# Kernel tuning notes

Measured on AMD Instinct MI355X. Metric: run time of the kernel, lower is better.

## Reference

```python
import jax, jax.numpy as jnp
import numpy as np

D_MODEL = 1024
NUM_HEADS = 16
D_K = D_MODEL // NUM_HEADS
D_FF = 4096
EPS = 1e-6


def setup_inputs() -> dict:
    key = jax.random.key(0)
    ks = jax.random.split(key, 12)
    B, S = 4, 1024
    s = 1.0 / np.sqrt(D_MODEL)
    return {
        "x": jax.random.normal(ks[0], (B, S, D_MODEL), dtype=jnp.float32),
        "ln1_g": jnp.ones((D_MODEL,), jnp.float32),
        "ln1_b": jnp.zeros((D_MODEL,), jnp.float32),
        "wq": jax.random.normal(ks[1], (D_MODEL, D_MODEL), jnp.float32) * s,
        "wk": jax.random.normal(ks[2], (D_MODEL, D_MODEL), jnp.float32) * s,
        "wv": jax.random.normal(ks[3], (D_MODEL, D_MODEL), jnp.float32) * s,
        "wo": jax.random.normal(ks[4], (D_MODEL, D_MODEL), jnp.float32) * s,
        "ln2_g": jnp.ones((D_MODEL,), jnp.float32),
        "ln2_b": jnp.zeros((D_MODEL,), jnp.float32),
        "w1": jax.random.normal(ks[5], (D_MODEL, D_FF), jnp.float32) * s,
        "b1": jnp.zeros((D_FF,), jnp.float32),
        "w2": jax.random.normal(ks[6], (D_FF, D_MODEL), jnp.float32) * (1.0 / np.sqrt(D_FF)),
        "b2": jnp.zeros((D_MODEL,), jnp.float32),
    }


def _layernorm(x, g, b):
    mu = jnp.mean(x, axis=-1, keepdims=True)
    var = jnp.var(x, axis=-1, keepdims=True)
    return (x - mu) * jax.lax.rsqrt(var + EPS) * g + b


def _mha(x, wq, wk, wv, wo):
    B, S, _ = x.shape
    # project and split heads: [B,S,D] -> [B,H,S,Dk]
    q = (x @ wq).reshape(B, S, NUM_HEADS, D_K).transpose(0, 2, 1, 3)
    k = (x @ wk).reshape(B, S, NUM_HEADS, D_K).transpose(0, 2, 1, 3)
    v = (x @ wv).reshape(B, S, NUM_HEADS, D_K).transpose(0, 2, 1, 3)
    scores = jnp.einsum("bhqd,bhkd->bhqk", q, k) / np.sqrt(D_K).astype(np.float32)
    attn = jax.nn.softmax(scores, axis=-1)  # no mask: source forwards mask=None
    out = jnp.einsum("bhqk,bhkd->bhqd", attn, v)
    out = out.transpose(0, 2, 1, 3).reshape(B, S, D_MODEL)
    return out @ wo


def reference(x, ln1_g, ln1_b, wq, wk, wv, wo, ln2_g, ln2_b, w1, b1, w2, b2):
    x1 = _layernorm(x, ln1_g, ln1_b)
    x = x + _mha(x1, wq, wk, wv, wo)  # dropout identity (eval)
    x2 = _layernorm(x, ln2_g, ln2_b)
    ffn = jax.nn.relu(x2 @ w1 + b1) @ w2 + b2
    return x + ffn
```

## Files before the change

### kernel.cpp

```cpp
#include <hip/hip_runtime.h>

typedef __bf16 bf16;
typedef __bf16 bf16x8 __attribute__((ext_vector_type(8)));
typedef __bf16 bf16x4 __attribute__((ext_vector_type(4)));
typedef float f32x4 __attribute__((ext_vector_type(4)));

__device__ __forceinline__ void gload_lds16(const void* g, void* l) {
  __builtin_amdgcn_global_load_lds(
      (const __attribute__((address_space(1))) unsigned int*)g,
      (__attribute__((address_space(3))) unsigned int*)l, 16, 0, 0);
}

__global__ __launch_bounds__(256) void transpose_cast(const float* __restrict__ src,
                                                      bf16* __restrict__ dst,
                                                      int R, int C) {
  __shared__ float tile[32][33];
  const int tx = threadIdx.x & 31, ty = threadIdx.x >> 5;
  const int c0 = blockIdx.x * 32, r0 = blockIdx.y * 32;
#pragma unroll
  for (int i = 0; i < 4; i++)
    tile[ty + i * 8][tx] = src[(size_t)(r0 + ty + i * 8) * C + c0 + tx];
  __syncthreads();
#pragma unroll
  for (int i = 0; i < 4; i++)
    dst[(size_t)(c0 + ty + i * 8) * R + r0 + tx] = (bf16)tile[tx][ty + i * 8];
}

__global__ __launch_bounds__(256) void ln_kernel(const float* __restrict__ x,
                                                 const float* __restrict__ g,
                                                 const float* __restrict__ b,
                                                 bf16* __restrict__ y) {
  const int w = threadIdx.x >> 6, lane = threadIdx.x & 63;
  const int row = blockIdx.x * 4 + w;
  const float* xr = x + (size_t)row * 1024;
  float4 v[4];
  float s = 0.f, sq = 0.f;
#pragma unroll
  for (int c = 0; c < 4; c++) {
    v[c] = *reinterpret_cast<const float4*>(xr + c * 256 + lane * 4);
    s += v[c].x + v[c].y + v[c].z + v[c].w;
    sq += v[c].x * v[c].x + v[c].y * v[c].y + v[c].z * v[c].z + v[c].w * v[c].w;
  }
#pragma unroll
  for (int d = 32; d >= 1; d >>= 1) {
    s += __shfl_xor(s, d, 64);
    sq += __shfl_xor(sq, d, 64);
  }
  const float mu = s * (1.f / 1024.f);
  const float rs = rsqrtf(sq * (1.f / 1024.f) - mu * mu + 1e-6f);
#pragma unroll
  for (int c = 0; c < 4; c++) {
    float4 gv = *reinterpret_cast<const float4*>(g + c * 256 + lane * 4);
    float4 bv = *reinterpret_cast<const float4*>(b + c * 256 + lane * 4);
    bf16x4 ov;
    ov[0] = (bf16)((v[c].x - mu) * rs * gv.x + bv.x);
    ov[1] = (bf16)((v[c].y - mu) * rs * gv.y + bv.y);
    ov[2] = (bf16)((v[c].z - mu) * rs * gv.z + bv.z);
    ov[3] = (bf16)((v[c].w - mu) * rs * gv.w + bv.w);
    *reinterpret_cast<bf16x4*>(y + (size_t)row * 1024 + c * 256 + lane * 4) = ov;
  }
}

__global__ __launch_bounds__(256) void reduce_ln_kernel(const bf16* __restrict__ p0,
                                                        const bf16* __restrict__ p1,
                                                        const float* __restrict__ x,
                                                        const float* __restrict__ g,
                                                        const float* __restrict__ b,
                                                        float* __restrict__ xres,
                                                        bf16* __restrict__ y) {
  const int w = threadIdx.x >> 6, lane = threadIdx.x & 63;
  const int row = blockIdx.x * 4 + w;
  const size_t rb = (size_t)row * 1024;
  float4 v[4];
  float s = 0.f, sq = 0.f;
#pragma unroll
  for (int c = 0; c < 4; c++) {
    const int off = c * 256 + lane * 4;
    float4 xv = *reinterpret_cast<const float4*>(x + rb + off);
    bf16x4 a0 = *reinterpret_cast<const bf16x4*>(p0 + rb + off);
    bf16x4 a1 = *reinterpret_cast<const bf16x4*>(p1 + rb + off);
    v[c].x = xv.x + (float)a0[0] + (float)a1[0];
    v[c].y = xv.y + (float)a0[1] + (float)a1[1];
    v[c].z = xv.z + (float)a0[2] + (float)a1[2];
    v[c].w = xv.w + (float)a0[3] + (float)a1[3];
    *reinterpret_cast<float4*>(xres + rb + off) = v[c];
    s += v[c].x + v[c].y + v[c].z + v[c].w;
    sq += v[c].x * v[c].x + v[c].y * v[c].y + v[c].z * v[c].z + v[c].w * v[c].w;
  }
#pragma unroll
  for (int d = 32; d >= 1; d >>= 1) {
    s += __shfl_xor(s, d, 64);
    sq += __shfl_xor(sq, d, 64);
  }
  const float mu = s * (1.f / 1024.f);
  const float rs = rsqrtf(sq * (1.f / 1024.f) - mu * mu + 1e-6f);
#pragma unroll
  for (int c = 0; c < 4; c++) {
    const int off = c * 256 + lane * 4;
    float4 gv = *reinterpret_cast<const float4*>(g + off);
    float4 bv = *reinterpret_cast<const float4*>(b + off);
    bf16x4 ov;
    ov[0] = (bf16)((v[c].x - mu) * rs * gv.x + bv.x);
    ov[1] = (bf16)((v[c].y - mu) * rs * gv.y + bv.y);
    ov[2] = (bf16)((v[c].z - mu) * rs * gv.z + bv.z);
    ov[3] = (bf16)((v[c].w - mu) * rs * gv.w + bv.w);
    *reinterpret_cast<bf16x4*>(y + rb + off) = ov;
  }
}

__global__ __launch_bounds__(256) void reduce_out_kernel(const bf16* __restrict__ p0,
                                                         const bf16* __restrict__ p1,
                                                         const bf16* __restrict__ p2,
                                                         const bf16* __restrict__ p3,
                                                         const float* __restrict__ bias,
                                                         const float* __restrict__ xres,
                                                         float* __restrict__ out) {
  const size_t i = ((size_t)blockIdx.x * 256 + threadIdx.x) * 8;
  const int col = (int)(i & 1023);
  bf16x8 a0 = *reinterpret_cast<const bf16x8*>(p0 + i);
  bf16x8 a1 = *reinterpret_cast<const bf16x8*>(p1 + i);
  bf16x8 a2 = *reinterpret_cast<const bf16x8*>(p2 + i);
  bf16x8 a3 = *reinterpret_cast<const bf16x8*>(p3 + i);
  float4 r0 = *reinterpret_cast<const float4*>(xres + i);
  float4 r1 = *reinterpret_cast<const float4*>(xres + i + 4);
  float4 b0 = *reinterpret_cast<const float4*>(bias + col);
  float4 b1 = *reinterpret_cast<const float4*>(bias + col + 4);
  float4 o0, o1;
  o0.x = r0.x + b0.x + (float)a0[0] + (float)a1[0] + (float)a2[0] + (float)a3[0];
  o0.y = r0.y + b0.y + (float)a0[1] + (float)a1[1] + (float)a2[1] + (float)a3[1];
  o0.z = r0.z + b0.z + (float)a0[2] + (float)a1[2] + (float)a2[2] + (float)a3[2];
  o0.w = r0.w + b0.w + (float)a0[3] + (float)a1[3] + (float)a2[3] + (float)a3[3];
  o1.x = r1.x + b1.x + (float)a0[4] + (float)a1[4] + (float)a2[4] + (float)a3[4];
  o1.y = r1.y + b1.y + (float)a0[5] + (float)a1[5] + (float)a2[5] + (float)a3[5];
  o1.z = r1.z + b1.z + (float)a0[6] + (float)a1[6] + (float)a2[6] + (float)a3[6];
  o1.w = r1.w + b1.w + (float)a0[7] + (float)a1[7] + (float)a2[7] + (float)a3[7];
  *reinterpret_cast<float4*>(out + i) = o0;
  *reinterpret_cast<float4*>(out + i + 4) = o1;
}

template <int EPI>
__global__ __launch_bounds__(256) void gemm_bt(const bf16* __restrict__ A,
                                               const bf16* __restrict__ Bt,
                                               void* __restrict__ Cout,
                                               const float* __restrict__ bias,
                                               int M, int N, int K, int gy, int gxy,
                                               int Kc) {
  __shared__ __align__(16) bf16 As[2][128][32];
  __shared__ __align__(16) bf16 Bs[2][128][32];
  const int tid = threadIdx.x;
  const int w = tid >> 6, lane = tid & 63;
  const int wr = w >> 1, wc = w & 1;

  const int nwg = gridDim.x;
  const int cpx = nwg >> 3;
  const int swz = (blockIdx.x & 7) * cpx + (blockIdx.x >> 3);
  const int chunk = swz / gxy, rem = swz % gxy;
  const int gpc = gy << 3;
  const int band = rem / gpc, r2 = rem % gpc;
  const int bm = (band * 8 + (r2 & 7)) * 128;
  const int bn = (r2 >> 3) * 128;

  f32x4 acc[4][4] = {};
  const int r4 = lane >> 2;
  const int c8 = (lane & 3) * 8;
  const bf16* Ag = A + (size_t)(bm + w * 32 + r4) * K + chunk * Kc + c8;
  const bf16* Bg = Bt + (size_t)(bn + w * 32 + r4) * K + chunk * Kc + c8;
  const int fr = lane & 15, fo = (lane >> 4) * 8;

#define STAGE(buf, k0)                                                 \
  do {                                                                 \
    gload_lds16(Ag + (k0), &As[buf][w * 32][0]);                       \
    gload_lds16(Ag + (size_t)16 * K + (k0), &As[buf][w * 32 + 16][0]); \
    gload_lds16(Bg + (k0), &Bs[buf][w * 32][0]);                       \
    gload_lds16(Bg + (size_t)16 * K + (k0), &Bs[buf][w * 32 + 16][0]); \
  } while (0)

  const int nt = Kc >> 5;
  STAGE(0, 0);
  __syncthreads();
  int cur = 0;
  for (int t = 0; t < nt; ++t) {
    if (t + 1 < nt) STAGE(cur ^ 1, (t + 1) << 5);
    bf16x8 af[4], bfr[4];
#pragma unroll
    for (int m = 0; m < 4; m++)
      af[m] = *reinterpret_cast<const bf16x8*>(&As[cur][wr * 64 + m * 16 + fr][fo]);
#pragma unroll
    for (int n = 0; n < 4; n++)
      bfr[n] = *reinterpret_cast<const bf16x8*>(&Bs[cur][wc * 64 + n * 16 + fr][fo]);
#pragma unroll
    for (int m = 0; m < 4; m++)
#pragma unroll
      for (int n = 0; n < 4; n++)
        acc[m][n] = __builtin_amdgcn_mfma_f32_16x16x32_bf16(af[m], bfr[n], acc[m][n], 0, 0, 0);
    __syncthreads();
    cur ^= 1;
  }
#undef STAGE

  bf16* outp = (bf16*)Cout + (EPI == 3 ? (size_t)chunk * M * N : 0);
  const int cr = (lane >> 4) * 4, cc = lane & 15;
#pragma unroll
  for (int m = 0; m < 4; m++) {
#pragma unroll
    for (int n = 0; n < 4; n++) {
      const int row = bm + wr * 64 + m * 16 + cr;
      const int col = bn + wc * 64 + n * 16 + cc;
#pragma unroll
      for (int r = 0; r < 4; r++) {
        const float va = acc[m][n][r];
        const size_t idx = (size_t)(row + r) * N + col;
        if (EPI == 0 || EPI == 3) {
          outp[idx] = (bf16)va;
        } else {
          const float t = va + bias[col];
          outp[idx] = (bf16)(t > 0.f ? t : 0.f);
        }
      }
    }
  }
}

template <int EPI>
__global__ __launch_bounds__(512, 2) void gemm256(const bf16* __restrict__ A,
                                                  const bf16* __restrict__ Bt,
                                                  void* __restrict__ Cout,
                                                  const float* __restrict__ bias,
                                                  int M, int N, int K, int gy, int gxy,
                                                  int Kc) {
  __shared__ __align__(16) bf16 As[2][256][64];
  __shared__ __align__(16) bf16 Bs[2][256][64];
  const int tid = threadIdx.x;
  const int w = tid >> 6, lane = tid & 63;
  const int wm = w >> 2, wn = w & 3;
  const int fr = lane & 15, g = lane >> 4;

  const int nwg = gridDim.x;
  const int cpx = nwg >> 3;
  const int swz = (blockIdx.x & 7) * cpx + (blockIdx.x >> 3);
  const int chunk = swz / gxy, rem = swz % gxy;
  const int gpc = gy << 3;
  const int band = rem / gpc, r2 = rem % gpc;
  const int bm = (band * 8 + (r2 & 7)) * 256;
  const int bn = (r2 >> 3) * 256;

  const bf16* Ab = A + (size_t)bm * K;
  const bf16* Bb = Bt + (size_t)bn * K;

  const int lr = lane >> 3;
  const int sle = ((lane & 7) ^ lr) * 8;
  const int rB0 = w * 16;
  const int rB1 = 128 + w * 16;
  const int rA0 = wm * 128 + wn * 16;
  const int rA1 = wm * 128 + 64 + wn * 16;

  char* AsB = (char*)&As[0][0][0];
  char* BsB = (char*)&Bs[0][0][0];
  const int rowA = (wm * 128 + fr) * 128;
  const int rowB = (wn * 64 + fr) * 128;
  const int colk0 = (g * 16) ^ ((fr & 7) << 4);
  const int colk1 = (64 + g * 16) ^ ((fr & 7) << 4);

  f32x4 acc[8][4] = {};

#define SG8(base, r0, kb, ldsrow)                                           \
  do {                                                                      \
    gload_lds16(base + (size_t)((r0) + lr) * K + (kb) + sle, (ldsrow));     \
    gload_lds16(base + (size_t)((r0) + 8 + lr) * K + (kb) + sle,            \
                (char*)(ldsrow) + 1024);                                    \
  } while (0)

  const int nt = Kc >> 6;
  const int koff = chunk * Kc;

  SG8(Bb, rB0, koff, BsB + rB0 * 128);
  SG8(Bb, rB1, koff, BsB + rB1 * 128);
  SG8(Ab, rA0, koff, AsB + rA0 * 128);
  SG8(Ab, rA1, koff, AsB + rA1 * 128);

#define PHASE_BODY(p, mb)                                                     \
  {                                                                           \
    if ((p) == 0) {                                                           \
      _Pragma("unroll") for (int nf = 0; nf < 4; nf++) {                      \
        bfr[nf][0] = *(const bf16x8*)(Br + rowB + nf * 2048 + colk0);         \
        bfr[nf][1] = *(const bf16x8*)(Br + rowB + nf * 2048 + colk1);         \
      }                                                                       \
    }                                                                         \
    af[0][0] = *(const bf16x8*)(Ar + rowA + (mb)*2048 + colk0);               \
    af[0][1] = *(const bf16x8*)(Ar + rowA + (mb)*2048 + colk1);               \
    af[1][0] = *(const bf16x8*)(Ar + rowA + ((mb) + 1) * 2048 + colk0);       \
    af[1][1] = *(const bf16x8*)(Ar + rowA + ((mb) + 1) * 2048 + colk1);       \
    if (pre) {                                                                \
      if ((p) == 0) SG8(Bb, rB0, kb2, Bw + rB0 * 128);                        \
      if ((p) == 1) SG8(Bb, rB1, kb2, Bw + rB1 * 128);                        \
      if ((p) == 2) SG8(Ab, rA0, kb2, Aw + rA0 * 128);                        \
      if ((p) == 3) SG8(Ab, rA1, kb2, Aw + rA1 * 128);                        \
    }                                                                         \
    __builtin_amdgcn_s_setprio(1);                                            \
    _Pragma("unroll") for (int m2 = 0; m2 < 2; m2++)                          \
        _Pragma("unroll") for (int nf = 0; nf < 4; nf++) {                    \
      acc[(mb) + m2][nf] = __builtin_amdgcn_mfma_f32_16x16x32_bf16(           \
          af[m2][0], bfr[nf][0], acc[(mb) + m2][nf], 0, 0, 0);                \
      acc[(mb) + m2][nf] = __builtin_amdgcn_mfma_f32_16x16x32_bf16(           \
          af[m2][1], bfr[nf][1], acc[(mb) + m2][nf], 0, 0, 0);                \
    }                                                                         \
    __builtin_amdgcn_s_setprio(0);                                            \
  }

  int buf = 0;
  for (int kt = 0; kt < nt; ++kt) {
    char* Ar = AsB + buf * 32768;
    char* Br = BsB + buf * 32768;
    char* Aw = AsB + (buf ^ 1) * 32768;
    char* Bw = BsB + (buf ^ 1) * 32768;
    const bool pre = (kt + 1) < nt;
    const int kb2 = koff + (kt + 1) * 64;
    bf16x8 bfr[4][2];
    bf16x8 af[2][2];

    asm volatile("s_waitcnt vmcnt(2)" ::: "memory");
    __builtin_amdgcn_s_barrier();
    PHASE_BODY(0, 0)

    if (pre) asm volatile("s_waitcnt vmcnt(4)" ::: "memory");
    else     asm volatile("s_waitcnt vmcnt(2)" ::: "memory");
    __builtin_amdgcn_s_barrier();
    PHASE_BODY(1, 2)

    if (pre) asm volatile("s_waitcnt vmcnt(4)" ::: "memory");
    else     asm volatile("s_waitcnt vmcnt(0)" ::: "memory");
    __builtin_amdgcn_s_barrier();
    PHASE_BODY(2, 4)

    if (pre) asm volatile("s_waitcnt vmcnt(6)" ::: "memory");
    else     asm volatile("s_waitcnt vmcnt(0)" ::: "memory");
    __builtin_amdgcn_s_barrier();
    PHASE_BODY(3, 6)

    buf ^= 1;
  }
#undef PHASE_BODY
#undef SG8

  bf16* outp = (bf16*)Cout + (EPI == 3 ? (size_t)chunk * M * N : 0);
  const int cr = g * 4;
#pragma unroll
  for (int mf = 0; mf < 8; mf++) {
#pragma unroll
    for (int nf = 0; nf < 4; nf++) {
      const int row = bm + wm * 128 + mf * 16 + cr;
      const int col = bn + wn * 64 + nf * 16 + fr;
#pragma unroll
      for (int r = 0; r < 4; r++) {
        const float va = acc[mf][nf][r];
        const size_t idx = (size_t)(row + r) * N + col;
        if (EPI == 3) {
          outp[idx] = (bf16)va;
        } else {
          const float t = va + bias[col];
          outp[idx] = (bf16)(t > 0.f ? t : 0.f);
        }
      }
    }
  }
}

__global__ __launch_bounds__(256) void attn_kernel(const bf16* __restrict__ Q,
                                                   const bf16* __restrict__ K,
                                                   const bf16* __restrict__ V,
                                                   bf16* __restrict__ O, int ld) {
  __shared__ __align__(16) bf16 Ks[2][64][64];
  __shared__ __align__(16) bf16 Vt[2][64][64];
  __shared__ __align__(16) bf16 Pl[4][32][64];
  const int tid = threadIdx.x;
  const int w = tid >> 6, l = tid & 63;
  const int lo = l & 15, g = l >> 4;
  const int sw = (lo & 7) << 3;

  const int id = blockIdx.x;
  const int bh = id & 63, qb = id >> 6;
  const int b = bh >> 4, h = bh & 15;
  const int hoff = h * 64;
  const size_t rowQ = (size_t)b * 1024 + qb * 128 + w * 32;
  const size_t rowKV0 = (size_t)b * 1024;

  bf16x8 qfr[2][2];
#pragma unroll
  for (int qi = 0; qi < 2; qi++)
#pragma unroll
    for (int ds = 0; ds < 2; ds++)
      qfr[qi][ds] = *reinterpret_cast<const bf16x8*>(
          Q + (rowQ + qi * 16 + lo) * ld + hoff + ds * 32 + g * 8);

  const float c = 0.18033688f;
  float m[2] = {-1e30f, -1e30f}, lsum[2] = {0.f, 0.f};
  f32x4 o[4][2] = {};

  {
#pragma unroll
    for (int i = 0; i < 2; i++) {
      const int idx = tid + i * 256;
      const int row = idx >> 3, cch = idx & 7;
      gload_lds16(K + (rowKV0 + row) * ld + hoff + ((cch ^ (row & 7)) << 3),
                  &Ks[0][row][cch << 3]);
    }
    const bf16* vp = V + (rowKV0 + l) * ld + hoff + w * 16;
    bf16x8 va = *reinterpret_cast<const bf16x8*>(vp);
    bf16x8 vb = *reinterpret_cast<const bf16x8*>(vp + 8);
#pragma unroll
    for (int j = 0; j < 8; j++) Vt[0][w * 16 + j][l ^ (j << 3)] = va[j];
#pragma unroll
    for (int j = 0; j < 8; j++) Vt[0][w * 16 + 8 + j][l ^ (j << 3)] = vb[j];
  }
  __syncthreads();

  int bb = 0;
  for (int kt = 0; kt < 16; kt++) {
    bf16x8 va, vb;
    const bool more = (kt + 1) < 16;
    if (more) {
      const size_t rkv = rowKV0 + (kt + 1) * 64;
#pragma unroll
      for (int i = 0; i < 2; i++) {
        const int idx = tid + i * 256;
        const int row = idx >> 3, cch = idx & 7;
        gload_lds16(K + (rkv + row) * ld + hoff + ((cch ^ (row & 7)) << 3),
                    &Ks[bb ^ 1][row][cch << 3]);
      }
      const bf16* vp = V + (rkv + l) * ld + hoff + w * 16;
      va = *reinterpret_cast<const bf16x8*>(vp);
      vb = *reinterpret_cast<const bf16x8*>(vp + 8);
    }

    f32x4 sa[4][2] = {};
#pragma unroll
    for (int ds = 0; ds < 2; ds++) {
      bf16x8 kf[4];
#pragma unroll
      for (int kfi = 0; kfi < 4; kfi++)
        kf[kfi] = *reinterpret_cast<const bf16x8*>(&Ks[bb][kfi * 16 + lo][(ds * 32 + g * 8) ^ sw]);
#pragma unroll
      for (int kfi = 0; kfi < 4; kfi++)
#pragma unroll
        for (int qi = 0; qi < 2; qi++)
          sa[kfi][qi] = __builtin_amdgcn_mfma_f32_16x16x32_bf16(kf[kfi], qfr[qi][ds], sa[kfi][qi], 0, 0, 0);
    }

#pragma unroll
    for (int qi = 0; qi < 2; qi++) {
      float m0 = fmaxf(fmaxf(sa[0][qi][0], sa[0][qi][1]), fmaxf(sa[0][qi][2], sa[0][qi][3]));
      float m1 = fmaxf(fmaxf(sa[1][qi][0], sa[1][qi][1]), fmaxf(sa[1][qi][2], sa[1][qi][3]));
      float m2 = fmaxf(fmaxf(sa[2][qi][0], sa[2][qi][1]), fmaxf(sa[2][qi][2], sa[2][qi][3]));
      float m3 = fmaxf(fmaxf(sa[3][qi][0], sa[3][qi][1]), fmaxf(sa[3][qi][2], sa[3][qi][3]));
      float mx = fmaxf(fmaxf(m0, m1), fmaxf(m2, m3));
      mx = fmaxf(mx, __shfl_xor(mx, 16));
      mx = fmaxf(mx, __shfl_xor(mx, 32));
      const float mn = fmaxf(m[qi], mx);
      const float sc = exp2f((m[qi] - mn) * c);
      const float mc = mn * c;
      m[qi] = mn;
      float p[16];
#pragma unroll
      for (int kfi = 0; kfi < 4; kfi++)
#pragma unroll
        for (int r = 0; r < 4; r++)
          p[kfi * 4 + r] = exp2f(fmaf(sa[kfi][qi][r], c, -mc));
      float s0 = (p[0] + p[1]) + (p[2] + p[3]);
      float s1 = (p[4] + p[5]) + (p[6] + p[7]);
      float s2 = (p[8] + p[9]) + (p[10] + p[11]);
      float s3 = (p[12] + p[13]) + (p[14] + p[15]);
      float sum = (s0 + s1) + (s2 + s3);
      sum += __shfl_xor(sum, 16);
      sum += __shfl_xor(sum, 32);
      lsum[qi] = lsum[qi] * sc + sum;
#pragma unroll
      for (int df = 0; df < 4; df++)
#pragma unroll
        for (int r = 0; r < 4; r++) o[df][qi][r] *= sc;
#pragma unroll
      for (int kfi = 0; kfi < 4; kfi++) {
        bf16x4 pk;
        pk[0] = (bf16)p[kfi * 4 + 0];
        pk[1] = (bf16)p[kfi * 4 + 1];
        pk[2] = (bf16)p[kfi * 4 + 2];
        pk[3] = (bf16)p[kfi * 4 + 3];
        *reinterpret_cast<bf16x4*>(&Pl[w][qi * 16 + lo][(kfi * 16 + g * 4) ^ sw]) = pk;
      }
    }

#pragma unroll
    for (int ks = 0; ks < 2; ks++) {
      bf16x8 pf[2], vf[4];
#pragma unroll
      for (int qi = 0; qi < 2; qi++)
        pf[qi] = *reinterpret_cast<const bf16x8*>(&Pl[w][qi * 16 + lo][(ks * 32 + g * 8) ^ sw]);
#pragma unroll
      for (int df = 0; df < 4; df++)
        vf[df] = *reinterpret_cast<const bf16x8*>(&Vt[bb][df * 16 + lo][(ks * 32 + g * 8) ^ sw]);
#pragma unroll
      for (int df = 0; df < 4; df++)
#pragma unroll
        for (int qi = 0; qi < 2; qi++)
          o[df][qi] = __builtin_amdgcn_mfma_f32_16x16x32_bf16(vf[df], pf[qi], o[df][qi], 0, 0, 0);
    }

    if (more) {
#pragma unroll
      for (int j = 0; j < 8; j++) Vt[bb ^ 1][w * 16 + j][l ^ (j << 3)] = va[j];
#pragma unroll
      for (int j = 0; j < 8; j++) Vt[bb ^ 1][w * 16 + 8 + j][l ^ (j << 3)] = vb[j];
    }
    __syncthreads();
    bb ^= 1;
  }

#pragma unroll
  for (int qi = 0; qi < 2; qi++) {
    const float rl = 1.f / lsum[qi];
#pragma unroll
    for (int df = 0; df < 4; df++) {
      bf16x4 ov;
#pragma unroll
      for (int r = 0; r < 4; r++) ov[r] = (bf16)(o[df][qi][r] * rl);
      *reinterpret_cast<bf16x4*>(&Pl[w][qi * 16 + lo][(df * 16 + g * 4) ^ sw]) = ov;
    }
  }
  const int row = l >> 1;
  const int swr = (row & 7) << 3;
#pragma unroll
  for (int i = 0; i < 4; i++) {
    const int c2 = (l & 1) * 4 + i;
    bf16x8 ov = *reinterpret_cast<const bf16x8*>(&Pl[w][row][(c2 * 8) ^ swr]);
    *reinterpret_cast<bf16x8*>(O + (rowQ + row) * 1024 + hoff + c2 * 8) = ov;
  }
}

extern "C" void kernel_launch(void* const* d_in, const int* in_sizes, int n_in,
                              void* d_out, int out_size, void* d_ws, size_t ws_size,
                              hipStream_t stream) {
  const float* x     = (const float*)d_in[0];
  const float* ln1_g = (const float*)d_in[1];
  const float* ln1_b = (const float*)d_in[2];
  const float* wq    = (const float*)d_in[3];
  const float* wk    = (const float*)d_in[4];
  const float* wv    = (const float*)d_in[5];
  const float* wo    = (const float*)d_in[6];
  const float* ln2_g = (const float*)d_in[7];
  const float* ln2_b = (const float*)d_in[8];
  const float* w1    = (const float*)d_in[9];
  const float* b1    = (const float*)d_in[10];
  const float* w2    = (const float*)d_in[11];
  const float* b2    = (const float*)d_in[12];

  const size_t MB = 1ull << 20;
  char* ws = (char*)d_ws;
  bf16* wTqkv = (bf16*)(ws + 0 * MB);
  bf16* wTo   = (bf16*)(ws + 6 * MB);
  bf16* wT1   = (bf16*)(ws + 8 * MB);
  bf16* wT2   = (bf16*)(ws + 16 * MB);
  bf16* x1    = (bf16*)(ws + 24 * MB);
  bf16* qkv   = (bf16*)(ws + 32 * MB);
  float* xres = (float*)(ws + 56 * MB);
  bf16* h1    = (bf16*)(ws + 72 * MB);
  bf16* attn  = x1;
  bf16* x2    = qkv;
  bf16* pOp   = (bf16*)(ws + 40 * MB);
  bf16* pF    = (bf16*)(ws + 24 * MB);

  const dim3 TB(256);

  transpose_cast<<<dim3(32, 32), TB, 0, stream>>>(wq, wTqkv, 1024, 1024);
  transpose_cast<<<dim3(32, 32), TB, 0, stream>>>(wk, wTqkv + 1024 * 1024, 1024, 1024);
  transpose_cast<<<dim3(32, 32), TB, 0, stream>>>(wv, wTqkv + 2048 * 1024, 1024, 1024);
  transpose_cast<<<dim3(32, 32), TB, 0, stream>>>(wo, wTo, 1024, 1024);
  transpose_cast<<<dim3(128, 32), TB, 0, stream>>>(w1, wT1, 1024, 4096);
  transpose_cast<<<dim3(32, 128), TB, 0, stream>>>(w2, wT2, 4096, 1024);

  ln_kernel<<<1024, TB, 0, stream>>>(x, ln1_g, ln1_b, x1);

  gemm_bt<0><<<768, TB, 0, stream>>>(x1, wTqkv, qkv, nullptr, 4096, 3072, 1024, 24, 768, 1024);

  attn_kernel<<<512, TB, 0, stream>>>(qkv, qkv + 1024, qkv + 2048, attn, 3072);

  gemm_bt<3><<<512, TB, 0, stream>>>(attn, wTo, pOp, nullptr, 4096, 1024, 1024, 8, 256, 512);

  reduce_ln_kernel<<<1024, TB, 0, stream>>>(pOp, pOp + 4096 * 1024, x, ln2_g, ln2_b, xres, x2);

  gemm256<2><<<256, dim3(512), 0, stream>>>(x2, wT1, h1, b1, 4096, 4096, 1024, 16, 256, 1024);

  gemm256<3><<<256, dim3(512), 0, stream>>>(h1, wT2, pF, nullptr, 4096, 1024, 4096, 4, 64, 1024);

  reduce_out_kernel<<<2048, TB, 0, stream>>>(pF, pF + 4096 * 1024, pF + 2 * 4096 * 1024,
                                             pF + 3 * 4096 * 1024, b2, xres, (float*)d_out);
}
```

Measured before the change: 219.9 us.

## Use 8 waves per attention block and skip unneeded softmax rescaling

Attention blocks now run 512 threads (8 waves), each wave handling 16 query rows instead of 32. The K/V tile loads are split across more threads and register pressure per wave drops, which is meant to raise occupancy and latency hiding. The online softmax also updates the running max and rescales the accumulators only when some lane's new max exceeds the stored one by more than a threshold. This saves the exp and multiply work in most iterations, but lets exponent arguments grow up to a bounded amount.

```diff
diff --git a/kernel.cpp b/kernel.cpp
--- a/kernel.cpp
+++ b/kernel.cpp
@@ -365,13 +365,13 @@
   }
 }
 
-__global__ __launch_bounds__(256) void attn_kernel(const bf16* __restrict__ Q,
-                                                   const bf16* __restrict__ K,
-                                                   const bf16* __restrict__ V,
-                                                   bf16* __restrict__ O, int ld) {
+__global__ __launch_bounds__(512, 4) void attn_kernel(const bf16* __restrict__ Q,
+                                                      const bf16* __restrict__ K,
+                                                      const bf16* __restrict__ V,
+                                                      bf16* __restrict__ O, int ld) {
   __shared__ __align__(16) bf16 Ks[2][64][64];
   __shared__ __align__(16) bf16 Vt[2][64][64];
-  __shared__ __align__(16) bf16 Pl[4][32][64];
+  __shared__ __align__(16) bf16 Pl[8][16][64];
   const int tid = threadIdx.x;
   const int w = tid >> 6, l = tid & 63;
   const int lo = l & 15, g = l >> 4;
@@ -381,58 +381,43 @@
   const int bh = id & 63, qb = id >> 6;
   const int b = bh >> 4, h = bh & 15;
   const int hoff = h * 64;
-  const size_t rowQ = (size_t)b * 1024 + qb * 128 + w * 32;
+  const size_t rowQ = (size_t)b * 1024 + qb * 128 + w * 16;
   const size_t rowKV0 = (size_t)b * 1024;
 
-  bf16x8 qfr[2][2];
-#pragma unroll
-  for (int qi = 0; qi < 2; qi++)
-#pragma unroll
-    for (int ds = 0; ds < 2; ds++)
-      qfr[qi][ds] = *reinterpret_cast<const bf16x8*>(
-          Q + (rowQ + qi * 16 + lo) * ld + hoff + ds * 32 + g * 8);
+  const int srow = tid >> 3, scch = tid & 7;
+  const int vcb = w * 8;
+
+  bf16x8 qfr[2];
+#pragma unroll
+  for (int ds = 0; ds < 2; ds++)
+    qfr[ds] = *reinterpret_cast<const bf16x8*>(
+        Q + (rowQ + lo) * ld + hoff + ds * 32 + g * 8);
 
   const float c = 0.18033688f;
-  float m[2] = {-1e30f, -1e30f}, lsum[2] = {0.f, 0.f};
-  f32x4 o[4][2] = {};
+  float m = -1e30f, lsum = 0.f;
+  f32x4 o[4] = {};
 
   {
-#pragma unroll
-    for (int i = 0; i < 2; i++) {
-      const int idx = tid + i * 256;
-      const int row = idx >> 3, cch = idx & 7;
-      gload_lds16(K + (rowKV0 + row) * ld + hoff + ((cch ^ (row & 7)) << 3),
-                  &Ks[0][row][cch << 3]);
-    }
-    const bf16* vp = V + (rowKV0 + l) * ld + hoff + w * 16;
-    bf16x8 va = *reinterpret_cast<const bf16x8*>(vp);
-    bf16x8 vb = *reinterpret_cast<const bf16x8*>(vp + 8);
-#pragma unroll
-    for (int j = 0; j < 8; j++) Vt[0][w * 16 + j][l ^ (j << 3)] = va[j];
-#pragma unroll
-    for (int j = 0; j < 8; j++) Vt[0][w * 16 + 8 + j][l ^ (j << 3)] = vb[j];
+    gload_lds16(K + (rowKV0 + srow) * ld + hoff + ((scch ^ (srow & 7)) << 3),
+                &Ks[0][w * 8][0]);
+    bf16x8 vv = *reinterpret_cast<const bf16x8*>(V + (rowKV0 + l) * ld + hoff + vcb);
+#pragma unroll
+    for (int j = 0; j < 8; j++) Vt[0][vcb + j][l ^ (j << 3)] = vv[j];
   }
   __syncthreads();
 
   int bb = 0;
   for (int kt = 0; kt < 16; kt++) {
-    bf16x8 va, vb;
+    bf16x8 vv;
     const bool more = (kt + 1) < 16;
     if (more) {
       const size_t rkv = rowKV0 + (kt + 1) * 64;
-#pragma unroll
-      for (int i = 0; i < 2; i++) {
-        const int idx = tid + i * 256;
-        const int row = idx >> 3, cch = idx & 7;
-        gload_lds16(K + (rkv + row) * ld + hoff + ((cch ^ (row & 7)) << 3),
-                    &Ks[bb ^ 1][row][cch << 3]);
-      }
-      const bf16* vp = V + (rkv + l) * ld + hoff + w * 16;
-      va = *reinterpret_cast<const bf16x8*>(vp);
-      vb = *reinterpret_cast<const bf16x8*>(vp + 8);
-    }
-
-    f32x4 sa[4][2] = {};
+      gload_lds16(K + (rkv + srow) * ld + hoff + ((scch ^ (srow & 7)) << 3),
+                  &Ks[bb ^ 1][w * 8][0]);
+      vv = *reinterpret_cast<const bf16x8*>(V + (rkv + l) * ld + hoff + vcb);
+    }
+
+    f32x4 sa[4] = {};
 #pragma unroll
     for (int ds = 0; ds < 2; ds++) {
       bf16x8 kf[4];
@@ -441,97 +426,84 @@
         kf[kfi] = *reinterpret_cast<const bf16x8*>(&Ks[bb][kfi * 16 + lo][(ds * 32 + g * 8) ^ sw]);
 #pragma unroll
       for (int kfi = 0; kfi < 4; kfi++)
-#pragma unroll
-        for (int qi = 0; qi < 2; qi++)
-          sa[kfi][qi] = __builtin_amdgcn_mfma_f32_16x16x32_bf16(kf[kfi], qfr[qi][ds], sa[kfi][qi], 0, 0, 0);
-    }
-
-#pragma unroll
-    for (int qi = 0; qi < 2; qi++) {
-      float m0 = fmaxf(fmaxf(sa[0][qi][0], sa[0][qi][1]), fmaxf(sa[0][qi][2], sa[0][qi][3]));
-      float m1 = fmaxf(fmaxf(sa[1][qi][0], sa[1][qi][1]), fmaxf(sa[1][qi][2], sa[1][qi][3]));
-      float m2 = fmaxf(fmaxf(sa[2][qi][0], sa[2][qi][1]), fmaxf(sa[2][qi][2], sa[2][qi][3]));
-      float m3 = fmaxf(fmaxf(sa[3][qi][0], sa[3][qi][1]), fmaxf(sa[3][qi][2], sa[3][qi][3]));
-      float mx = fmaxf(fmaxf(m0, m1), fmaxf(m2, m3));
-      mx = fmaxf(mx, __shfl_xor(mx, 16));
-      mx = fmaxf(mx, __shfl_xor(mx, 32));
-      const float mn = fmaxf(m[qi], mx);
-      const float sc = exp2f((m[qi] - mn) * c);
-      const float mc = mn * c;
-      m[qi] = mn;
-      float p[16];
-#pragma unroll
-      for (int kfi = 0; kfi < 4; kfi++)
-#pragma unroll
-        for (int r = 0; r < 4; r++)
-          p[kfi * 4 + r] = exp2f(fmaf(sa[kfi][qi][r], c, -mc));
-      float s0 = (p[0] + p[1]) + (p[2] + p[3]);
-      float s1 = (p[4] + p[5]) + (p[6] + p[7]);
-      float s2 = (p[8] + p[9]) + (p[10] + p[11]);
-      float s3 = (p[12] + p[13]) + (p[14] + p[15]);
-      float sum = (s0 + s1) + (s2 + s3);
-      sum += __shfl_xor(sum, 16);
-      sum += __shfl_xor(sum, 32);
-      lsum[qi] = lsum[qi] * sc + sum;
+        sa[kfi] = __builtin_amdgcn_mfma_f32_16x16x32_bf16(kf[kfi], qfr[ds], sa[kfi], 0, 0, 0);
+    }
+
+    float m0 = fmaxf(fmaxf(sa[0][0], sa[0][1]), fmaxf(sa[0][2], sa[0][3]));
+    float m1 = fmaxf(fmaxf(sa[1][0], sa[1][1]), fmaxf(sa[1][2], sa[1][3]));
+    float m2 = fmaxf(fmaxf(sa[2][0], sa[2][1]), fmaxf(sa[2][2], sa[2][3]));
+    float m3 = fmaxf(fmaxf(sa[3][0], sa[3][1]), fmaxf(sa[3][2], sa[3][3]));
+    float mx = fmaxf(fmaxf(m0, m1), fmaxf(m2, m3));
+    mx = fmaxf(mx, __shfl_xor(mx, 16));
+    mx = fmaxf(mx, __shfl_xor(mx, 32));
+    if (__any(mx - m > 16.f)) {
+      const float mn = fmaxf(m, mx);
+      const float sc = exp2f((m - mn) * c);
+      lsum *= sc;
 #pragma unroll
       for (int df = 0; df < 4; df++)
 #pragma unroll
-        for (int r = 0; r < 4; r++) o[df][qi][r] *= sc;
-#pragma unroll
-      for (int kfi = 0; kfi < 4; kfi++) {
-        bf16x4 pk;
-        pk[0] = (bf16)p[kfi * 4 + 0];
-        pk[1] = (bf16)p[kfi * 4 + 1];
-        pk[2] = (bf16)p[kfi * 4 + 2];
-        pk[3] = (bf16)p[kfi * 4 + 3];
-        *reinterpret_cast<bf16x4*>(&Pl[w][qi * 16 + lo][(kfi * 16 + g * 4) ^ sw]) = pk;
+        for (int r = 0; r < 4; r++) o[df][r] *= sc;
+      m = mn;
+    }
+    const float mc = m * c;
+    float p[16];
+#pragma unroll
+    for (int kfi = 0; kfi < 4; kfi++)
+#pragma unroll
+      for (int r = 0; r < 4; r++)
+        p[kfi * 4 + r] = exp2f(fmaf(sa[kfi][r], c, -mc));
+    float s0 = (p[0] + p[1]) + (p[2] + p[3]);
+    float s1 = (p[4] + p[5]) + (p[6] + p[7]);
+    float s2 = (p[8] + p[9]) + (p[10] + p[11]);
+    float s3 = (p[12] + p[13]) + (p[14] + p[15]);
+    float sum = (s0 + s1) + (s2 + s3);
+    sum += __shfl_xor(sum, 16);
+    sum += __shfl_xor(sum, 32);
+    lsum += sum;
+#pragma unroll
+    for (int kfi = 0; kfi < 4; kfi++) {
+      bf16x4 pk;
+      pk[0] = (bf16)p[kfi * 4 + 0];
+      pk[1] = (bf16)p[kfi * 4 + 1];
+      pk[2] = (bf16)p[kfi * 4 + 2];
+      pk[3] = (bf16)p[kfi * 4 + 3];
+      *reinterpret_cast<bf16x4*>(&Pl[w][lo][(kfi * 16 + g * 4) ^ sw]) = pk;
+    }
+
+#pragma unroll
+    for (int ks = 0; ks < 2; ks++) {
+      bf16x8 pf = *reinterpret_cast<const bf16x8*>(&Pl[w][lo][(ks * 32 + g * 8) ^ sw]);
+#pragma unroll
+      for (int df = 0; df < 4; df++) {
+        bf16x8 vf = *reinterpret_cast<const bf16x8*>(&Vt[bb][df * 16 + lo][(ks * 32 + g * 8) ^ sw]);
+        o[df] = __builtin_amdgcn_mfma_f32_16x16x32_bf16(vf, pf, o[df], 0, 0, 0);
       }
     }
 
-#pragma unroll
-    for (int ks = 0; ks < 2; ks++) {
-      bf16x8 pf[2], vf[4];
-#pragma unroll
-      for (int qi = 0; qi < 2; qi++)
-        pf[qi] = *reinterpret_cast<const bf16x8*>(&Pl[w][qi * 16 + lo][(ks * 32 + g * 8) ^ sw]);
-#pragma unroll
-      for (int df = 0; df < 4; df++)
-        vf[df] = *reinterpret_cast<const bf16x8*>(&Vt[bb][df * 16 + lo][(ks * 32 + g * 8) ^ sw]);
-#pragma unroll
-      for (int df = 0; df < 4; df++)
-#pragma unroll
-        for (int qi = 0; qi < 2; qi++)
-          o[df][qi] = __builtin_amdgcn_mfma_f32_16x16x32_bf16(vf[df], pf[qi], o[df][qi], 0, 0, 0);
-    }
-
     if (more) {
 #pragma unroll
-      for (int j = 0; j < 8; j++) Vt[bb ^ 1][w * 16 + j][l ^ (j << 3)] = va[j];
-#pragma unroll
-      for (int j = 0; j < 8; j++) Vt[bb ^ 1][w * 16 + 8 + j][l ^ (j << 3)] = vb[j];
+      for (int j = 0; j < 8; j++) Vt[bb ^ 1][vcb + j][l ^ (j << 3)] = vv[j];
     }
     __syncthreads();
     bb ^= 1;
   }
 
-#pragma unroll
-  for (int qi = 0; qi < 2; qi++) {
-    const float rl = 1.f / lsum[qi];
-#pragma unroll
-    for (int df = 0; df < 4; df++) {
-      bf16x4 ov;
-#pragma unroll
-      for (int r = 0; r < 4; r++) ov[r] = (bf16)(o[df][qi][r] * rl);
-      *reinterpret_cast<bf16x4*>(&Pl[w][qi * 16 + lo][(df * 16 + g * 4) ^ sw]) = ov;
-    }
-  }
-  const int row = l >> 1;
+  const float rl = 1.f / lsum;
+#pragma unroll
+  for (int df = 0; df < 4; df++) {
+    bf16x4 ov;
+#pragma unroll
+    for (int r = 0; r < 4; r++) ov[r] = (bf16)(o[df][r] * rl);
+    *reinterpret_cast<bf16x4*>(&Pl[w][lo][(df * 16 + g * 4) ^ sw]) = ov;
+  }
+  const int row = l >> 2;
   const int swr = (row & 7) << 3;
-#pragma unroll
-  for (int i = 0; i < 4; i++) {
-    const int c2 = (l & 1) * 4 + i;
-    bf16x8 ov = *reinterpret_cast<const bf16x8*>(&Pl[w][row][(c2 * 8) ^ swr]);
-    *reinterpret_cast<bf16x8*>(O + (rowQ + row) * 1024 + hoff + c2 * 8) = ov;
+  const int c2 = (l & 3) * 16;
+#pragma unroll
+  for (int i = 0; i < 2; i++) {
+    bf16x8 ov = *reinterpret_cast<const bf16x8*>(&Pl[w][row][(c2 + i * 8) ^ swr]);
+    *reinterpret_cast<bf16x8*>(O + (rowQ + row) * 1024 + hoff + c2 + i * 8) = ov;
   }
 }
 
@@ -580,7 +552,7 @@
 
   gemm_bt<0><<<768, TB, 0, stream>>>(x1, wTqkv, qkv, nullptr, 4096, 3072, 1024, 24, 768, 1024);
 
-  attn_kernel<<<512, TB, 0, stream>>>(qkv, qkv + 1024, qkv + 2048, attn, 3072);
+  attn_kernel<<<512, dim3(512), 0, stream>>>(qkv, qkv + 1024, qkv + 2048, attn, 3072);
 
   gemm_bt<3><<<512, TB, 0, stream>>>(attn, wTo, pOp, nullptr, 4096, 1024, 1024, 8, 256, 512);
 
```

Result: no change. 217.0 us (-1.3%).
